# Kernel optimization log

Measured on AMD Instinct MI355X. Metric: run time of the kernel, lower is better.

Reference implementation:

```python
import jax, jax.numpy as jnp
import numpy as np

GROUPS = 32
EPS = 1e-5
NUM_HEADS = 16


def group_norm(x, gamma, beta):
    # x: [b, c, s]; GroupNorm over (c//G, s) per group, affine per channel
    b, c, s = x.shape
    xg = x.reshape(b, GROUPS, (c // GROUPS) * s)
    mean = xg.mean(axis=-1, keepdims=True)
    var = xg.var(axis=-1, keepdims=True)
    xn = ((xg - mean) * jax.lax.rsqrt(var + EPS)).reshape(b, c, s)
    return xn * gamma[None, :, None] + beta[None, :, None]


def setup_inputs() -> dict:
    key = jax.random.key(0)
    ks = jax.random.split(key, 8)
    b, c, H, W = 16, 1024, 32, 32
    ctx_dim, Sk = 2048, 256
    x = jax.random.normal(ks[0], (b, c, H, W), jnp.float32)
    context = jax.random.normal(ks[1], (b, Sk, ctx_dim), jnp.float32)
    mask = jax.random.randint(ks[2], (b, Sk), 0, 2, jnp.int32)
    gamma_x = jnp.ones((c,), jnp.float32)
    beta_x = jnp.zeros((c,), jnp.float32)
    gamma_c = jnp.ones((ctx_dim,), jnp.float32)
    beta_c = jnp.zeros((ctx_dim,), jnp.float32)
    Wq = jax.random.normal(ks[3], (c, c), jnp.float32) * (1.0 / np.sqrt(c))
    bq = jnp.zeros((c,), jnp.float32)
    Wkv = jax.random.normal(ks[4], (2 * c, ctx_dim), jnp.float32) * (1.0 / np.sqrt(ctx_dim))
    bkv = jnp.zeros((2 * c,), jnp.float32)
    # proj_out is zero-initialized in the original (zero_module); use small random
    # weights so the attention path contributes to the output / gradients.
    Wp = jax.random.normal(ks[5], (c, c), jnp.float32) * (0.02 / np.sqrt(c))
    bp = jnp.zeros((c,), jnp.float32)
    return {"x": x, "context": context, "mask": mask,
            "gamma_x": gamma_x, "beta_x": beta_x, "gamma_c": gamma_c, "beta_c": beta_c,
            "Wq": Wq, "bq": bq, "Wkv": Wkv, "bkv": bkv, "Wp": Wp, "bp": bp}


def reference(x, context, mask, gamma_x, beta_x, gamma_c, beta_c, Wq, bq, Wkv, bkv, Wp, bp):
    b, c = x.shape[0], x.shape[1]
    spatial = x.shape[2:]
    xf = x.reshape(b, c, -1)                       # [b, c, Sq]
    Sq = xf.shape[-1]
    h_heads = NUM_HEADS
    d = c // h_heads

    # q = conv1x1(GroupNorm(x))
    q = jnp.einsum('oc,bcs->bos', Wq, group_norm(xf, gamma_x, beta_x)) + bq[None, :, None]
    # context -> [b, ctx_dim, Sk], GroupNorm, kv conv1x1
    ctx = jnp.transpose(context, (0, 2, 1))
    ctx_n = group_norm(ctx, gamma_c, beta_c)
    kv = jnp.einsum('oc,bcs->bos', Wkv, ctx_n) + bkv[None, :, None]  # [b, 2c, Sk]
    k, v = kv[:, :c], kv[:, c:]

    # QKVStableMaskedAttention: scale q and k each by 1/sqrt(sqrt(d))
    scale = 1.0 / np.sqrt(np.sqrt(d))
    qh = (q * scale).reshape(b, h_heads, d, Sq)
    kh = (k * scale).reshape(b, h_heads, d, -1)
    vh = v.reshape(b, h_heads, d, -1)
    w = jnp.einsum('bhdt,bhds->bhts', qh, kh)      # [b, h, Sq, Sk]
    mbool = mask.astype(bool)[:, None, None, :]
    w = jnp.where(mbool, w, jnp.float32(-1e9))
    w = jax.nn.softmax(w, axis=-1)                 # stable softmax (max-subtracted)
    a = jnp.einsum('bhts,bhds->bhdt', w, vh).reshape(b, c, Sq)

    h_out = jnp.einsum('oc,bcs->bos', Wp, a) + bp[None, :, None]
    return (xf + h_out).reshape(b, c, *spatial)
```

## Files before the change

### kernel.cpp

```cpp
#include <hip/hip_runtime.h>
#include <stdint.h>

#define DEV static __device__ __forceinline__

typedef unsigned short u16;
typedef u16  u16x8 __attribute__((ext_vector_type(8)));
typedef u16  u16x4 __attribute__((ext_vector_type(4)));
typedef float f32x4 __attribute__((ext_vector_type(4)));
typedef short s16x8 __attribute__((ext_vector_type(8)));

#define BB 16
#define CC 1024
#define SS 1024
#define CTX 2048
#define SKK 256
#define NH 16
#define HD 64
#define NG 32
#define ATT_SCALE 0.35355339059327373f

DEV u16 f2bf(float f) {
  uint32_t u = __float_as_uint(f);
  return (u16)((u + 0x7fffu + ((u >> 16) & 1u)) >> 16);
}
DEV s16x8 ld8(const u16* p) { return __builtin_bit_cast(s16x8, *(const u16x8*)p); }
DEV f32x4 zero4() { f32x4 z = {0.f, 0.f, 0.f, 0.f}; return z; }

DEV void gload_lds16(const void* g, const void* l) {
  __builtin_amdgcn_global_load_lds(
      (const __attribute__((address_space(1))) unsigned int*)(uintptr_t)g,
      (__attribute__((address_space(3))) unsigned int*)(uint32_t)(uintptr_t)l,
      16, 0, 0);
}

__global__ __launch_bounds__(256) void prep_misc(const float* __restrict__ Wq,
                                                 const float* __restrict__ Wkv,
                                                 const float* __restrict__ Wp,
                                                 const int* __restrict__ mask,
                                                 u16* __restrict__ wq_bf,
                                                 u16* __restrict__ wkv_bf,
                                                 u16* __restrict__ wp_bf,
                                                 float* __restrict__ mb) {
  const int bid = blockIdx.x, tid = threadIdx.x;
  const float* src; u16* dst; int i;
  if (bid < 1024)      { src = Wq;  dst = wq_bf;  i = bid * 256 + tid; }
  else if (bid < 5120) { src = Wkv; dst = wkv_bf; i = (bid - 1024) * 256 + tid; }
  else if (bid < 6144) { src = Wp;  dst = wp_bf;  i = (bid - 5120) * 256 + tid; }
  else {
    int j = (bid - 6144) * 256 + tid;
    mb[j] = mask[j] ? 0.f : -1e9f;
    return;
  }
  f32x4 v = ((const f32x4*)src)[i];
  u16x4 o; o[0]=f2bf(v[0]); o[1]=f2bf(v[1]); o[2]=f2bf(v[2]); o[3]=f2bf(v[3]);
  ((u16x4*)dst)[i] = o;
}

__global__ __launch_bounds__(256) void gn_stats_all(const float* __restrict__ x,
                                                    const float* __restrict__ ctx,
                                                    float* __restrict__ stx,
                                                    float* __restrict__ stc) {
  const int bid = blockIdx.x, tid = threadIdx.x;
  float s = 0.f, ss = 0.f;
  float* st; int slot; float inv_n;
  if (bid < 512) {
    const int b = bid >> 5, g = bid & 31;
    const float* p = x + ((size_t)b * CC + g * 32) * SS;
    for (int it = 0; it < 32; ++it) {
      f32x4 v = *(const f32x4*)(p + it * 1024 + tid * 4);
      s  += v[0] + v[1] + v[2] + v[3];
      ss += v[0]*v[0] + v[1]*v[1] + v[2]*v[2] + v[3]*v[3];
    }
    st = stx; slot = bid; inv_n = 1.f / 32768.f;
  } else {
    const int bid2 = bid - 512;
    const int b = bid2 >> 5, g = bid2 & 31;
    const float* p = ctx + (size_t)b * SKK * CTX + g * 64;
    const int ch = tid & 63, r0 = tid >> 6;
    for (int it = 0; it < 64; ++it) {
      float v = p[(size_t)(it * 4 + r0) * CTX + ch];
      s += v; ss += v * v;
    }
    st = stc; slot = bid2; inv_n = 1.f / 16384.f;
  }
  __shared__ float red[512];
  red[tid] = s; red[256 + tid] = ss;
  __syncthreads();
  for (int o = 128; o > 0; o >>= 1) {
    if (tid < o) { red[tid] += red[tid + o]; red[256 + tid] += red[256 + tid + o]; }
    __syncthreads();
  }
  if (tid == 0) {
    float mean = red[0] * inv_n;
    float var  = red[256] * inv_n - mean * mean;
    st[slot * 2 + 0] = mean;
    st[slot * 2 + 1] = rsqrtf(var + 1e-5f);
  }
}

__global__ __launch_bounds__(256) void gn_apply_all(const float* __restrict__ x,
                                                    const float* __restrict__ ctx,
                                                    const float* __restrict__ stx,
                                                    const float* __restrict__ stc,
                                                    const float* __restrict__ gamma_x,
                                                    const float* __restrict__ beta_x,
                                                    const float* __restrict__ gamma_c,
                                                    const float* __restrict__ beta_c,
                                                    u16* __restrict__ xnT,
                                                    u16* __restrict__ ctxn) {
  __shared__ float t[64][65];
  const int bid = blockIdx.x, tid = threadIdx.x;
  if (bid < 8192) {
    size_t i = ((size_t)bid * 256 + tid) * 4;
    int ch = (int)(i & 2047);
    int bs = (int)(i >> 11);
    int b = bs >> 8;
    int g = ch >> 6;
    float mean = stc[(b * 32 + g) * 2], rstd = stc[(b * 32 + g) * 2 + 1];
    f32x4 v  = *(const f32x4*)(ctx + i);
    f32x4 ga = *(const f32x4*)(gamma_c + ch);
    f32x4 be = *(const f32x4*)(beta_c + ch);
    u16x4 o;
    o[0] = f2bf((v[0] - mean) * rstd * ga[0] + be[0]);
    o[1] = f2bf((v[1] - mean) * rstd * ga[1] + be[1]);
    o[2] = f2bf((v[2] - mean) * rstd * ga[2] + be[2]);
    o[3] = f2bf((v[3] - mean) * rstd * ga[3] + be[3]);
    *(u16x4*)(ctxn + i) = o;
    return;
  }
  const int id2 = bid - 8192;
  const int b = id2 >> 8, c0 = ((id2 >> 4) & 15) * 64, s0 = (id2 & 15) * 64;
  const int j = tid & 63, i0 = tid >> 6;
  for (int it = 0; it < 16; ++it) {
    int i = it * 4 + i0;
    int c = c0 + i;
    int g = c >> 5;
    float mean = stx[(b * 32 + g) * 2], rstd = stx[(b * 32 + g) * 2 + 1];
    float v = x[((size_t)b * CC + c) * SS + s0 + j];
    t[i][j] = (v - mean) * rstd * gamma_x[c] + beta_x[c];
  }
  __syncthreads();
  for (int it = 0; it < 16; ++it) {
    int jj = it * 4 + i0;
    xnT[((size_t)b * SS + s0 + jj) * CC + c0 + j] = f2bf(t[j][jj]);
  }
}

DEV void gemm8_core(const u16* __restrict__ A, const u16* __restrict__ B,
                    int ld, int nu, u16* lds, f32x4 acc[8][4], int tid) {
  const int wid = tid >> 6, lane = tid & 63;
  const int wr = wid >> 2, wc = wid & 3;
  const int fr = lane & 15, hi = lane >> 4;
  const int rj0 = tid >> 2, kk = (tid & 3) * 8;

  auto STAGE = [&](int u) {
    int uc = u < nu ? u : nu - 1;
    int kof = (uc >> 1) * 64 + (uc & 1) * 32 + kk;
    u16* la = lds + (u & 3) * 16384;
    gload_lds16(A + (long)rj0 * ld + kof,         la + tid * 8);
    gload_lds16(A + (long)(rj0 + 128) * ld + kof, la + 4096 + tid * 8);
    gload_lds16(B + (long)rj0 * ld + kof,         la + 8192 + tid * 8);
    gload_lds16(B + (long)(rj0 + 128) * ld + kof, la + 12288 + tid * 8);
  };

  STAGE(0); STAGE(1); STAGE(2);

#pragma unroll 1
  for (int g = 0; g < nu; ++g) {
    asm volatile("s_waitcnt vmcnt(8)" ::: "memory");
    __builtin_amdgcn_s_barrier();
    __builtin_amdgcn_sched_barrier(0);
    const u16* As = lds + (g & 3) * 16384;
    const u16* Bs = As + 8192;
    s16x8 a[8], b[4];
#pragma unroll
    for (int m = 0; m < 8; ++m) a[m] = ld8(As + (wr * 128 + m * 16 + fr) * 32 + hi * 8);
#pragma unroll
    for (int n = 0; n < 4; ++n) b[n] = ld8(Bs + (wc * 64 + n * 16 + fr) * 32 + hi * 8);
    STAGE(g + 3);
    __builtin_amdgcn_s_setprio(1);
#pragma unroll
    for (int m = 0; m < 8; ++m)
#pragma unroll
      for (int n = 0; n < 4; ++n)
        acc[m][n] = __builtin_amdgcn_mfma_f32_16x16x32_bf16(a[m], b[n], acc[m][n], 0, 0, 0);
    __builtin_amdgcn_s_setprio(0);
  }
}

__global__ __launch_bounds__(512) void gemm_qkv8(
    const u16* __restrict__ xnT, const u16* __restrict__ wq,
    const u16* __restrict__ ctxn, const u16* __restrict__ wkv,
    u16* __restrict__ qt, u16* __restrict__ kvt, u16* __restrict__ v2,
    const float* __restrict__ bq, const float* __restrict__ bkv) {
  __shared__ alignas(16) u16 lds[65536];
  const int tid = threadIdx.x;
  const int xcd = blockIdx.x & 7, l = blockIdx.x >> 3;
  const int wid = tid >> 6, lane = tid & 63;
  const int wr = wid >> 2, wc = wid & 3;
  const int fr = lane & 15, hi = lane >> 4;

  f32x4 acc[8][4];
#pragma unroll
  for (int m = 0; m < 8; ++m)
#pragma unroll
    for (int n = 0; n < 4; ++n) acc[m][n] = zero4();

  if (l < 16) {
    const int kvid = xcd * 16 + l;
    const int bz = kvid >> 3, tn = kvid & 7;
    const u16* A = ctxn + (long)bz * SKK * CTX;
    const u16* B = wkv + (long)tn * 256 * CTX;
    gemm8_core(A, B, CTX, 64, lds, acc, tid);

    const int rowb = wr * 128 + hi * 4;
    const int colb = tn * 256 + wc * 64 + fr;
    if (tn < 4) {
      u16* C = kvt + (long)bz * SKK * CTX;
#pragma unroll
      for (int m = 0; m < 8; ++m)
#pragma unroll
        for (int n = 0; n < 4; ++n) {
          int col = colb + n * 16;
          float bia = bkv[col];
          f32x4 vv = acc[m][n];
#pragma unroll
          for (int i = 0; i < 4; ++i)
            C[(long)(rowb + m * 16 + i) * CTX + col] = f2bf((vv[i] + bia) * ATT_SCALE);
        }
    } else {
      u16* V = v2 + (long)bz * CC * SKK;
#pragma unroll
      for (int m = 0; m < 8; ++m)
#pragma unroll
        for (int n = 0; n < 4; ++n) {
          int col = colb + n * 16;
          float bia = bkv[col];
          f32x4 vv = acc[m][n];
          u16x4 pk;
#pragma unroll
          for (int i = 0; i < 4; ++i) pk[i] = f2bf(vv[i] + bia);
          *(u16x4*)(V + (long)(col - CC) * SKK + rowb + m * 16) = pk;
        }
    }
  } else {
    const int q = xcd * 32 + (l - 16);
    const int bz = q >> 4, tm = (q >> 2) & 3, tn = q & 3;
    const u16* A = xnT + (long)bz * SS * CC + (long)tm * 256 * CC;
    const u16* B = wq + (long)tn * 256 * CC;
    gemm8_core(A, B, CC, 32, lds, acc, tid);

    u16* C = qt + (long)bz * SS * CC;
    const int rowb = tm * 256 + wr * 128 + hi * 4;
    const int colb = tn * 256 + wc * 64 + fr;
#pragma unroll
    for (int m = 0; m < 8; ++m)
#pragma unroll
      for (int n = 0; n < 4; ++n) {
        int col = colb + n * 16;
        float bia = bq[col];
        f32x4 vv = acc[m][n];
#pragma unroll
        for (int i = 0; i < 4; ++i)
          C[(long)(rowb + m * 16 + i) * CC + col] = f2bf((vv[i] + bia) * ATT_SCALE);
      }
  }
}

__global__ __launch_bounds__(512) void gemm_proj8(
    const u16* __restrict__ wp, const u16* __restrict__ at,
    float* __restrict__ out, const float* __restrict__ bp,
    const float* __restrict__ x) {
  __shared__ alignas(16) u16 lds[65536];
  const int tid = threadIdx.x;
  const int v = (blockIdx.x & 7) * 32 + (blockIdx.x >> 3);
  const int bz = v >> 4, tm = (v >> 2) & 3, tn = v & 3;
  const int wid = tid >> 6, lane = tid & 63;
  const int wr = wid >> 2, wc = wid & 3;
  const int fr = lane & 15, hi = lane >> 4;

  f32x4 acc[8][4];
#pragma unroll
  for (int m = 0; m < 8; ++m)
#pragma unroll
    for (int n = 0; n < 4; ++n) acc[m][n] = zero4();

  const u16* A = wp + (long)tm * 256 * CC;
  const u16* B = at + (long)bz * SS * CC + (long)tn * 256 * CC;
  gemm8_core(A, B, CC, 32, lds, acc, tid);

  float* C = out + (long)bz * CC * SS;
  const float* R = x + (long)bz * CC * SS;
  const int rowb = tm * 256 + wr * 128 + hi * 4;
  const int colb = tn * 256 + wc * 64 + fr;
#pragma unroll
  for (int m = 0; m < 8; ++m)
#pragma unroll
    for (int n = 0; n < 4; ++n) {
      int col = colb + n * 16;
      f32x4 vv = acc[m][n];
#pragma unroll
      for (int i = 0; i < 4; ++i) {
        int row = rowb + m * 16 + i;
        long idx = (long)row * SS + col;
        C[idx] = R[idx] + vv[i] + bp[row];
      }
    }
}

__global__ __launch_bounds__(256) void attn_fused(const u16* __restrict__ qt,
                                                  const u16* __restrict__ kvt,
                                                  const u16* __restrict__ v2,
                                                  const float* __restrict__ mbias,
                                                  u16* __restrict__ at) {
  __shared__ alignas(16) u16 k_lds[256 * 64];
  __shared__ alignas(16) u16 v_lds[64 * 256];
  const int orig = blockIdx.x + 16 * blockIdx.y + 256 * blockIdx.z;
  const int v = (orig & 7) * 512 + (orig >> 3);
  const int bb = v >> 8, h = (v >> 4) & 15, t0 = (v & 15) * 64;

  const int tid = threadIdx.x, wid = tid >> 6, lane = tid & 63;
  const int fr = lane & 15, hi = lane >> 4;
  const int sw = fr & 7;

#pragma unroll
  for (int it = 0; it < 8; ++it) {
    int lin = (wid * 8 + it) * 1024 + lane * 16;
    int kr = lin >> 7, kc = (lin >> 4) & 7;
    gload_lds16(kvt + ((long)bb * SKK + kr) * CTX + h * HD + ((kc ^ (kr & 7)) << 3),
                (const char*)k_lds + (wid * 8 + it) * 1024);
    int vr = lin >> 9, vc = (lin >> 4) & 31;
    gload_lds16(v2 + ((long)bb * CC + h * HD + vr) * SKK + ((vc ^ (vr & 7)) << 3),
                (const char*)v_lds + (wid * 8 + it) * 1024);
  }

  const u16* qp = qt + ((long)bb * SS + t0 + wid * 16 + fr) * CC + h * HD + hi * 8;
  s16x8 aq0 = ld8(qp), aq1 = ld8(qp + 32);

  __syncthreads();

  f32x4 sc[16];
#pragma unroll
  for (int nf = 0; nf < 16; ++nf) {
    const u16* krow = k_lds + (nf * 16 + fr) * 64;
    s16x8 kb0 = ld8(krow + (((hi) ^ sw) << 3));
    s16x8 kb1 = ld8(krow + (((4 + hi) ^ sw) << 3));
    f32x4 z = zero4();
    z = __builtin_amdgcn_mfma_f32_16x16x32_bf16(aq0, kb0, z, 0, 0, 0);
    sc[nf] = __builtin_amdgcn_mfma_f32_16x16x32_bf16(aq1, kb1, z, 0, 0, 0);
  }

  __syncthreads();

  const float* mb = mbias + bb * SKK + fr;
#pragma unroll
  for (int nf = 0; nf < 16; ++nf) sc[nf] = sc[nf] + mb[nf * 16];

#pragma unroll
  for (int i = 0; i < 4; ++i) {
    float m = sc[0][i];
#pragma unroll
    for (int nf = 1; nf < 16; ++nf) m = fmaxf(m, sc[nf][i]);
#pragma unroll
    for (int d = 1; d < 16; d <<= 1) m = fmaxf(m, __shfl_xor(m, d));
    float s = 0.f;
#pragma unroll
    for (int nf = 0; nf < 16; ++nf) {
      float e = __expf(sc[nf][i] - m);
      sc[nf][i] = e; s += e;
    }
#pragma unroll
    for (int d = 1; d < 16; d <<= 1) s += __shfl_xor(s, d);
    float inv = 1.0f / s;
#pragma unroll
    for (int nf = 0; nf < 16; ++nf) sc[nf][i] *= inv;
  }

  u16* p_base = k_lds + wid * 4096;
#pragma unroll
  for (int nf = 0; nf < 16; ++nf) {
    int c = 2 * nf + (fr >> 3);
#pragma unroll
    for (int i = 0; i < 4; ++i) {
      int t = 4 * hi + i;
      p_base[t * 256 + (((c ^ (t & 7)) << 3)) + sw] = f2bf(sc[nf][i]);
    }
  }

  f32x4 ov[4];
#pragma unroll
  for (int n = 0; n < 4; ++n) ov[n] = zero4();
#pragma unroll
  for (int kk = 0; kk < 8; ++kk) {
    int c = 4 * kk + hi;
    s16x8 pa = ld8(p_base + fr * 256 + ((c ^ sw) << 3));
#pragma unroll
    for (int n = 0; n < 4; ++n) {
      int o = n * 16 + fr;
      s16x8 vb = ld8(v_lds + o * 256 + ((c ^ sw) << 3));
      ov[n] = __builtin_amdgcn_mfma_f32_16x16x32_bf16(pa, vb, ov[n], 0, 0, 0);
    }
  }

  const int rbase = hi * 4;
  u16* po = at + ((long)bb * SS + t0 + wid * 16 + rbase) * CC + h * HD + fr;
#pragma unroll
  for (int n = 0; n < 4; ++n)
#pragma unroll
    for (int i = 0; i < 4; ++i) po[(long)i * CC + n * 16] = f2bf(ov[n][i]);
}

extern "C" void kernel_launch(void* const* d_in, const int* in_sizes, int n_in,
                              void* d_out, int out_size, void* d_ws, size_t ws_size,
                              hipStream_t stream) {
  const float* x       = (const float*)d_in[0];
  const float* context = (const float*)d_in[1];
  const int*   mask    = (const int*)d_in[2];
  const float* gamma_x = (const float*)d_in[3];
  const float* beta_x  = (const float*)d_in[4];
  const float* gamma_c = (const float*)d_in[5];
  const float* beta_c  = (const float*)d_in[6];
  const float* Wq      = (const float*)d_in[7];
  const float* bq      = (const float*)d_in[8];
  const float* Wkv     = (const float*)d_in[9];
  const float* bkv     = (const float*)d_in[10];
  const float* Wp      = (const float*)d_in[11];
  const float* bp      = (const float*)d_in[12];
  float* out = (float*)d_out;

  char* w = (char*)d_ws;
  size_t off = 0;
  u16* wq_bf  = (u16*)(w + off); off += (size_t)CC * CC * 2;
  u16* wkv_bf = (u16*)(w + off); off += (size_t)CTX * CTX * 2;
  u16* wp_bf  = (u16*)(w + off); off += (size_t)CC * CC * 2;
  u16* xnT    = (u16*)(w + off); off += (size_t)BB * SS * CC * 2;
  u16* ctxn   = (u16*)(w + off); off += (size_t)BB * SKK * CTX * 2;
  u16* qt     = (u16*)(w + off); off += (size_t)BB * SS * CC * 2;
  u16* kvt    = (u16*)(w + off); off += (size_t)BB * SKK * CTX * 2;
  u16* v2     = (u16*)(w + off); off += (size_t)BB * CC * SKK * 2;
  u16* at     = (u16*)(w + off); off += (size_t)BB * SS * CC * 2;
  float* mb   = (float*)(w + off); off += (size_t)BB * SKK * 4;
  float* stx  = (float*)(w + off); off += (size_t)BB * NG * 2 * 4;
  float* stc  = (float*)(w + off); off += (size_t)BB * NG * 2 * 4;
  (void)ws_size; (void)in_sizes; (void)n_in; (void)out_size;

  prep_misc<<<6160, 256, 0, stream>>>(Wq, Wkv, Wp, mask, wq_bf, wkv_bf, wp_bf, mb);

  gn_stats_all<<<1024, 256, 0, stream>>>(x, context, stx, stc);

  gn_apply_all<<<12288, 256, 0, stream>>>(x, context, stx, stc,
                                          gamma_x, beta_x, gamma_c, beta_c,
                                          xnT, ctxn);

  gemm_qkv8<<<384, 512, 0, stream>>>(xnT, wq_bf, ctxn, wkv_bf, qt, kvt, v2, bq, bkv);

  attn_fused<<<dim3(16, NH, BB), 256, 0, stream>>>(qt, kvt, v2, mb, at);

  gemm_proj8<<<256, 512, 0, stream>>>(wp_bf, at, out, bp, x);
}
```

Baseline: 389.9 us.

## Merge prep and stats kernels, swizzle GEMM LDS, prefetch fragments across iterations

Folds the weight-conversion/mask kernel and the GroupNorm stats kernel into one launch, removing a launch boundary. In the shared GEMM core, the k-offset of each 16-byte chunk is XOR-swizzled by row in both global-to-LDS staging and fragment reads, to reduce LDS bank conflicts. The loop is restructured so the LDS fragment reads for the next stage are issued after the MFMAs of the current one, overlapping LDS latency with compute. This adds a barrier per iteration, and the stage-reuse distance needs care to avoid races.

```diff
diff --git a/kernel.cpp b/kernel.cpp
--- a/kernel.cpp
+++ b/kernel.cpp
@@ -33,55 +33,56 @@
       16, 0, 0);
 }
 
-__global__ __launch_bounds__(256) void prep_misc(const float* __restrict__ Wq,
-                                                 const float* __restrict__ Wkv,
-                                                 const float* __restrict__ Wp,
-                                                 const int* __restrict__ mask,
-                                                 u16* __restrict__ wq_bf,
-                                                 u16* __restrict__ wkv_bf,
-                                                 u16* __restrict__ wp_bf,
-                                                 float* __restrict__ mb) {
+__global__ __launch_bounds__(256) void prep_stats(const float* __restrict__ Wq,
+                                                  const float* __restrict__ Wkv,
+                                                  const float* __restrict__ Wp,
+                                                  const int* __restrict__ mask,
+                                                  const float* __restrict__ x,
+                                                  const float* __restrict__ ctx,
+                                                  u16* __restrict__ wq_bf,
+                                                  u16* __restrict__ wkv_bf,
+                                                  u16* __restrict__ wp_bf,
+                                                  float* __restrict__ mb,
+                                                  float* __restrict__ stx,
+                                                  float* __restrict__ stc) {
   const int bid = blockIdx.x, tid = threadIdx.x;
-  const float* src; u16* dst; int i;
-  if (bid < 1024)      { src = Wq;  dst = wq_bf;  i = bid * 256 + tid; }
-  else if (bid < 5120) { src = Wkv; dst = wkv_bf; i = (bid - 1024) * 256 + tid; }
-  else if (bid < 6144) { src = Wp;  dst = wp_bf;  i = (bid - 5120) * 256 + tid; }
-  else {
-    int j = (bid - 6144) * 256 + tid;
-    mb[j] = mask[j] ? 0.f : -1e9f;
+  if (bid < 6160) {
+    const float* src; u16* dst; int i;
+    if (bid < 1024)      { src = Wq;  dst = wq_bf;  i = bid * 256 + tid; }
+    else if (bid < 5120) { src = Wkv; dst = wkv_bf; i = (bid - 1024) * 256 + tid; }
+    else if (bid < 6144) { src = Wp;  dst = wp_bf;  i = (bid - 5120) * 256 + tid; }
+    else {
+      int j = (bid - 6144) * 256 + tid;
+      mb[j] = mask[j] ? 0.f : -1e9f;
+      return;
+    }
+    f32x4 v = ((const f32x4*)src)[i];
+    u16x4 o; o[0]=f2bf(v[0]); o[1]=f2bf(v[1]); o[2]=f2bf(v[2]); o[3]=f2bf(v[3]);
+    ((u16x4*)dst)[i] = o;
     return;
   }
-  f32x4 v = ((const f32x4*)src)[i];
-  u16x4 o; o[0]=f2bf(v[0]); o[1]=f2bf(v[1]); o[2]=f2bf(v[2]); o[3]=f2bf(v[3]);
-  ((u16x4*)dst)[i] = o;
-}
-
-__global__ __launch_bounds__(256) void gn_stats_all(const float* __restrict__ x,
-                                                    const float* __restrict__ ctx,
-                                                    float* __restrict__ stx,
-                                                    float* __restrict__ stc) {
-  const int bid = blockIdx.x, tid = threadIdx.x;
+  const int sid = bid - 6160;
   float s = 0.f, ss = 0.f;
   float* st; int slot; float inv_n;
-  if (bid < 512) {
-    const int b = bid >> 5, g = bid & 31;
+  if (sid < 512) {
+    const int b = sid >> 5, g = sid & 31;
     const float* p = x + ((size_t)b * CC + g * 32) * SS;
     for (int it = 0; it < 32; ++it) {
       f32x4 v = *(const f32x4*)(p + it * 1024 + tid * 4);
       s  += v[0] + v[1] + v[2] + v[3];
       ss += v[0]*v[0] + v[1]*v[1] + v[2]*v[2] + v[3]*v[3];
     }
-    st = stx; slot = bid; inv_n = 1.f / 32768.f;
+    st = stx; slot = sid; inv_n = 1.f / 32768.f;
   } else {
-    const int bid2 = bid - 512;
-    const int b = bid2 >> 5, g = bid2 & 31;
+    const int sid2 = sid - 512;
+    const int b = sid2 >> 5, g = sid2 & 31;
     const float* p = ctx + (size_t)b * SKK * CTX + g * 64;
     const int ch = tid & 63, r0 = tid >> 6;
     for (int it = 0; it < 64; ++it) {
       float v = p[(size_t)(it * 4 + r0) * CTX + ch];
       s += v; ss += v * v;
     }
-    st = stc; slot = bid2; inv_n = 1.f / 16384.f;
+    st = stc; slot = sid2; inv_n = 1.f / 16384.f;
   }
   __shared__ float red[512];
   red[tid] = s; red[256 + tid] = ss;
@@ -151,11 +152,13 @@
   const int wid = tid >> 6, lane = tid & 63;
   const int wr = wid >> 2, wc = wid & 3;
   const int fr = lane & 15, hi = lane >> 4;
-  const int rj0 = tid >> 2, kk = (tid & 3) * 8;
+  const int rj0 = tid >> 2;
+  const int ksw = (((tid & 3) ^ ((rj0 >> 1) & 3)) << 3);
+  const int ko  = ((hi ^ ((fr >> 1) & 3)) << 3);
 
   auto STAGE = [&](int u) {
     int uc = u < nu ? u : nu - 1;
-    int kof = (uc >> 1) * 64 + (uc & 1) * 32 + kk;
+    int kof = (uc >> 1) * 64 + (uc & 1) * 32 + ksw;
     u16* la = lds + (u & 3) * 16384;
     gload_lds16(A + (long)rj0 * ld + kof,         la + tid * 8);
     gload_lds16(A + (long)(rj0 + 128) * ld + kof, la + 4096 + tid * 8);
@@ -163,21 +166,27 @@
     gload_lds16(B + (long)(rj0 + 128) * ld + kof, la + 12288 + tid * 8);
   };
 
+  s16x8 a[8], b[4];
+  auto READS = [&](int g) {
+    const u16* As = lds + (g & 3) * 16384;
+    const u16* Bs = As + 8192;
+#pragma unroll
+    for (int m = 0; m < 8; ++m) a[m] = ld8(As + (wr * 128 + m * 16 + fr) * 32 + ko);
+#pragma unroll
+    for (int n = 0; n < 4; ++n) b[n] = ld8(Bs + (wc * 64 + n * 16 + fr) * 32 + ko);
+  };
+
   STAGE(0); STAGE(1); STAGE(2);
+  asm volatile("s_waitcnt vmcnt(8)" ::: "memory");
+  __builtin_amdgcn_s_barrier();
+  READS(0);
 
 #pragma unroll 1
   for (int g = 0; g < nu; ++g) {
-    asm volatile("s_waitcnt vmcnt(8)" ::: "memory");
+    STAGE(g + 3);
     __builtin_amdgcn_s_barrier();
+    asm volatile("s_waitcnt lgkmcnt(0)" ::: "memory");
     __builtin_amdgcn_sched_barrier(0);
-    const u16* As = lds + (g & 3) * 16384;
-    const u16* Bs = As + 8192;
-    s16x8 a[8], b[4];
-#pragma unroll
-    for (int m = 0; m < 8; ++m) a[m] = ld8(As + (wr * 128 + m * 16 + fr) * 32 + hi * 8);
-#pragma unroll
-    for (int n = 0; n < 4; ++n) b[n] = ld8(Bs + (wc * 64 + n * 16 + fr) * 32 + hi * 8);
-    STAGE(g + 3);
     __builtin_amdgcn_s_setprio(1);
 #pragma unroll
     for (int m = 0; m < 8; ++m)
@@ -185,6 +194,9 @@
       for (int n = 0; n < 4; ++n)
         acc[m][n] = __builtin_amdgcn_mfma_f32_16x16x32_bf16(a[m], b[n], acc[m][n], 0, 0, 0);
     __builtin_amdgcn_s_setprio(0);
+    asm volatile("s_waitcnt vmcnt(8)" ::: "memory");
+    __builtin_amdgcn_s_barrier();
+    if (g + 1 < nu) READS(g + 1);
   }
 }
 
@@ -444,9 +456,8 @@
   float* stc  = (float*)(w + off); off += (size_t)BB * NG * 2 * 4;
   (void)ws_size; (void)in_sizes; (void)n_in; (void)out_size;
 
-  prep_misc<<<6160, 256, 0, stream>>>(Wq, Wkv, Wp, mask, wq_bf, wkv_bf, wp_bf, mb);
-
-  gn_stats_all<<<1024, 256, 0, stream>>>(x, context, stx, stc);
+  prep_stats<<<7184, 256, 0, stream>>>(Wq, Wkv, Wp, mask, x, context,
+                                       wq_bf, wkv_bf, wp_bf, mb, stx, stc);
 
   gn_apply_all<<<12288, 256, 0, stream>>>(x, context, stx, stc,
                                           gamma_x, beta_x, gamma_c, beta_c,
```

New measurement: 386.4 us. No clear change (-0.9%).
